# Optimization experiments

Hardware: AMD Instinct MI355X
Metric: run time of the kernel (lower is better)

Reference implementation:

```python
import jax, jax.numpy as jnp
import numpy as np

BG_ID = 0
RADIUS = 10
MODE = 'gauss'
LAMBDA_B = 1.0
GAMMA = 0.1
TEMP = 4.0
EPS = 1e-8
BIG = 1e6  # stands in for +inf (no fg in a row/column); BIG**2 is fp32-safe


def setup_inputs() -> dict:
    key = jax.random.key(0)
    k1, k2 = jax.random.split(key)
    B, C, H, W = 4, 19, 256, 256
    return {
        'student_logits': jax.random.normal(k1, (B, C, H, W), jnp.float32),
        'teacher_logits': jax.random.normal(k2, (B, C, H, W), jnp.float32),
    }


def _edt2(fg):
    """Exact squared Euclidean distance transform of (1 - fg):
    distance from each pixel to the nearest foreground pixel.
    Separable algorithm: 1D column pass (two cumulative scans), then
    exact lower-envelope minimization along rows (vectorized brute force).
    fg: bool [B, H, W]. Returns float32 [B, H, W]."""
    B, H, W = fg.shape
    ii = jnp.arange(H, dtype=jnp.float32)[None, :, None]  # row index
    # 1D vertical distance to nearest fg pixel in each column
    d_fwd = ii - jax.lax.cummax(jnp.where(fg, ii, -BIG), axis=1)
    d_bwd = -jax.lax.cummax(jnp.where(fg, -ii, -BIG), axis=1, reverse=True) - ii
    g = jnp.minimum(jnp.minimum(d_fwd, d_bwd), BIG)  # [B,H,W]
    # exact 2D squared EDT: dist2[b,i,j] = min_{j'} (j-j')^2 + g[b,i,j']^2
    jj = jnp.arange(W, dtype=jnp.float32)
    diff2 = (jj[:, None] - jj[None, :]) ** 2  # [W, W']
    dist2 = jnp.min(diff2[None, None, :, :] + (g * g)[:, :, None, :], axis=-1)
    return dist2


def _erode(fg):
    """scipy.ndimage.binary_erosion with 4-connected cross structure and
    border_value=0 (out-of-bounds treated as background)."""
    p = jnp.pad(fg, ((0, 0), (1, 1), (1, 1)))
    return fg & p[:, :-2, 1:-1] & p[:, 2:, 1:-1] & p[:, 1:-1, :-2] & p[:, 1:-1, 2:]


def _weight_map(teacher_logits):
    # argmax of softmax(probs) == argmax of logits (softmax is monotone per-pixel)
    pred = jnp.argmax(teacher_logits, axis=1)  # [B,H,W]
    fg = pred != BG_ID
    dist2 = _edt2(fg)
    dist = jnp.sqrt(dist2)
    mask = (dist <= RADIUS).astype(jnp.float32)
    sigma = RADIUS / 2.0
    if MODE == 'gauss':
        wdist = jnp.exp(-dist2 / (2.0 * sigma * sigma))
    else:
        wdist = jnp.clip(1.0 - dist / RADIUS, 0.0, 1.0)
    wdist = wdist * mask
    boundary = (fg & ~_erode(fg)).astype(jnp.float32)
    # wb = wdist*(1+lambda_b*boundary); final weights = wb*mask_inside
    # (if an image has no fg pixels, dist is huge -> mask==0 -> weights==0,
    #  matching the scipy loop's `continue` which leaves zeros)
    return wdist * (1.0 + LAMBDA_B * boundary) * mask


def reference(student_logits, teacher_logits):
    weight_map = _weight_map(teacher_logits)  # [B,H,W]
    # teacher probs at temperature T (torch computes t_prob_T and t_prob
    # identically twice; computed once here)
    t_prob = jax.nn.softmax(teacher_logits / TEMP, axis=1)
    entropy = -jnp.sum(t_prob * jnp.log(jnp.clip(t_prob, EPS, None)), axis=1)
    ent_max = jnp.max(entropy, axis=(1, 2), keepdims=True)
    conf_factor = GAMMA + (1.0 - GAMMA) * (1.0 - entropy / (ent_max + EPS))
    s_logp = jax.nn.log_softmax(student_logits / TEMP, axis=1)
    kl_per_pixel = jnp.sum(t_prob * (jnp.log(t_prob + EPS) - s_logp), axis=1)
    total_weight = weight_map * conf_factor
    loss = jnp.sum(total_weight * kl_per_pixel) / (jnp.sum(total_weight) + EPS)
    return TEMP * TEMP * loss
```

## Files before the change

### kernel.cpp

```cpp
#include <hip/hip_runtime.h>
#include <math.h>

#define NC   19
#define HH   256
#define WW   256
#define NB   4
#define HW   (HH * WW)
#define NPIX (NB * HW)
#define CAP2 121.0f

__global__ __launch_bounds__(256) void k_pixel(
    const float* __restrict__ student, const float* __restrict__ teacher,
    float* __restrict__ entropy, float* __restrict__ kl,
    unsigned char* __restrict__ fg, float* __restrict__ bmax)
{
    const int p = blockIdx.x * 256 + threadIdx.x;
    const int b = p >> 16;
    const int r = p & (HW - 1);
    const float* tb = teacher + (size_t)b * NC * HW + r;
    const float* sb = student + (size_t)b * NC * HW + r;

    float St = 0.f, T1 = 0.f, T2 = 0.f, Ss = 0.f;
    float tmx = -INFINITY;
    int ax = 0;
#pragma unroll
    for (int c = 0; c < NC; ++c) {
        float tv = tb[(size_t)c * HW];
        float sv = sb[(size_t)c * HW];
        if (tv > tmx) { tmx = tv; ax = c; }
        float e = __expf(tv * 0.25f);
        St += e;
        T1 += e * tv;
        T2 += e * sv;
        Ss += __expf(sv * 0.25f);
    }
    float rSt = 1.0f / St;
    float ent = __logf(St) - 0.25f * T1 * rSt;
    float klv = __logf(Ss) - 0.25f * T2 * rSt - ent;

    entropy[p] = ent;
    kl[p]      = klv;
    fg[p]      = (ax != 0) ? 1 : 0;

    float m = ent;
#pragma unroll
    for (int o = 32; o >= 1; o >>= 1) m = fmaxf(m, __shfl_down(m, o, 64));
    __shared__ float red[4];
    int wave = threadIdx.x >> 6, lane = threadIdx.x & 63;
    if (lane == 0) red[wave] = m;
    __syncthreads();
    if (threadIdx.x == 0)
        bmax[blockIdx.x] = fmaxf(fmaxf(red[0], red[1]), fmaxf(red[2], red[3]));
}

#define TS   32
#define HALO 10
#define FW   (TS + 2 * HALO)

__global__ __launch_bounds__(256) void k_tile(
    const unsigned char* __restrict__ fg, const float* __restrict__ entropy,
    const float* __restrict__ kl, const float* __restrict__ bmax,
    double* __restrict__ part)
{
    __shared__ float  fgt[FW][FW];
    __shared__ float  vm[TS][FW];
    __shared__ float  red[4];
    __shared__ double snum[4], sden[4];

    const int b   = blockIdx.z;
    const int ti0 = blockIdx.y * TS;
    const int tj0 = blockIdx.x * TS;
    const int tid = threadIdx.x;
    const int wave = tid >> 6, lane = tid & 63;
    const unsigned char* fgb = fg + (size_t)b * HW;

    float m = bmax[(b << 8) + tid];
#pragma unroll
    for (int o = 32; o >= 1; o >>= 1) m = fmaxf(m, __shfl_down(m, o, 64));
    if (lane == 0) red[wave] = m;

    for (int l = tid; l < FW * FW; l += 256) {
        int li = l / FW, lj = l - li * FW;
        int gi = ti0 - HALO + li, gj = tj0 - HALO + lj;
        float v = 0.f;
        if (gi >= 0 && gi < HH && gj >= 0 && gj < WW) v = (float)fgb[gi * WW + gj];
        fgt[li][lj] = v;
    }
    __syncthreads();
    float em = fmaxf(fmaxf(red[0], red[1]), fmaxf(red[2], red[3]));

    for (int l = tid; l < TS * FW; l += 256) {
        int i = l / FW, jj = l - i * FW;
        float mn = CAP2;
#pragma unroll
        for (int di = -HALO; di <= HALO; ++di) {
            float fv = fgt[HALO + i + di][jj];
            mn = fminf(mn, (float)(di * di) + (1.0f - fv) * 1000.0f);
        }
        vm[i][jj] = mn;
    }
    __syncthreads();

    double num = 0.0, den = 0.0;
#pragma unroll
    for (int k = 0; k < (TS * TS) / 256; ++k) {
        int p = tid + k * 256;
        int i = p >> 5, j = p & (TS - 1);
        float d2 = CAP2;
#pragma unroll
        for (int dj = -HALO; dj <= HALO; ++dj)
            d2 = fminf(d2, (float)(dj * dj) + vm[i][j + HALO + dj]);
        float mask  = (d2 <= 100.0f) ? 1.0f : 0.0f;
        float wdist = __expf(-d2 * 0.02f) * mask;

        float f  = fgt[HALO + i][HALO + j];
        float up = fgt[HALO + i - 1][HALO + j];
        float dn = fgt[HALO + i + 1][HALO + j];
        float lf = fgt[HALO + i][HALO + j - 1];
        float rt = fgt[HALO + i][HALO + j + 1];
        float mn4 = fminf(fminf(up, dn), fminf(lf, rt));
        float boundary = (f != 0.f && mn4 == 0.f) ? 1.0f : 0.0f;

        float w = wdist * (1.0f + boundary) * mask;
        size_t gidx = (size_t)b * HW + (size_t)(ti0 + i) * WW + (tj0 + j);
        float conf = 0.1f + 0.9f * (1.0f - entropy[gidx] / (em + 1e-8f));
        float tw = w * conf;
        num += (double)(tw * kl[gidx]);
        den += (double)tw;
    }

#pragma unroll
    for (int o = 32; o >= 1; o >>= 1) {
        num += __shfl_down(num, o, 64);
        den += __shfl_down(den, o, 64);
    }
    if (lane == 0) { snum[wave] = num; sden[wave] = den; }
    __syncthreads();
    if (tid == 0) {
        int bid = (blockIdx.z << 6) + (blockIdx.y << 3) + blockIdx.x;
        part[bid * 2 + 0] = snum[0] + snum[1] + snum[2] + snum[3];
        part[bid * 2 + 1] = sden[0] + sden[1] + sden[2] + sden[3];
    }
}

__global__ __launch_bounds__(256) void k_final(
    const double* __restrict__ part, float* __restrict__ out)
{
    const int tid = threadIdx.x;
    double num = part[tid * 2 + 0];
    double den = part[tid * 2 + 1];
#pragma unroll
    for (int o = 32; o >= 1; o >>= 1) {
        num += __shfl_down(num, o, 64);
        den += __shfl_down(den, o, 64);
    }
    __shared__ double snum[4], sden[4];
    int wave = tid >> 6, lane = tid & 63;
    if (lane == 0) { snum[wave] = num; sden[wave] = den; }
    __syncthreads();
    if (tid == 0) {
        num = snum[0] + snum[1] + snum[2] + snum[3];
        den = sden[0] + sden[1] + sden[2] + sden[3];
        out[0] = (float)(16.0 * num / (den + 1e-8));
    }
}

extern "C" void kernel_launch(void* const* d_in, const int* in_sizes, int n_in,
                              void* d_out, int out_size, void* d_ws, size_t ws_size,
                              hipStream_t stream)
{
    const float* student = (const float*)d_in[0];
    const float* teacher = (const float*)d_in[1];
    float* out = (float*)d_out;

    char* ws = (char*)d_ws;
    double*        part    = (double*)(ws + 0);
    float*         bmax    = (float*)(ws + 8192);
    float*         entropy = (float*)(ws + 16384);
    float*         kl      = (float*)(ws + 16384 + (size_t)NPIX * 4);
    unsigned char* fg      = (unsigned char*)(ws + 16384 + (size_t)NPIX * 8);

    k_pixel<<<NPIX / 256, 256, 0, stream>>>(student, teacher, entropy, kl, fg, bmax);
    dim3 g2(WW / TS, HH / TS, NB);
    k_tile<<<g2, 256, 0, stream>>>(fg, entropy, kl, bmax, part);
    k_final<<<1, 256, 0, stream>>>(part, out);
}
```

Baseline: 88.48 us.

## Vectorize pixel kernel to float4 and widen tile kernel to 512 threads

The per-pixel softmax/KL kernel now has each thread process four adjacent pixels through float4 loads and stores and a uchar4 foreground write, cutting the thread count and issuing wider memory transactions. The tile kernel moves to 512 threads per block, which raises parallelism within its 256 blocks. Its per-image entropy max becomes a single-wave xor-shuffle over the 64 block maxima, removing a shared-memory exchange. Per-thread register use in the pixel kernel grows, which may reduce occupancy there.

```diff
diff --git a/kernel.cpp b/kernel.cpp
--- a/kernel.cpp
+++ b/kernel.cpp
@@ -7,47 +7,68 @@
 #define NB   4
 #define HW   (HH * WW)
 #define NPIX (NB * HW)
+#define NQ   (NPIX / 4)
+#define CHQ  (HW / 4)
 #define CAP2 121.0f
 
 __global__ __launch_bounds__(256) void k_pixel(
-    const float* __restrict__ student, const float* __restrict__ teacher,
-    float* __restrict__ entropy, float* __restrict__ kl,
-    unsigned char* __restrict__ fg, float* __restrict__ bmax)
-{
-    const int p = blockIdx.x * 256 + threadIdx.x;
-    const int b = p >> 16;
-    const int r = p & (HW - 1);
-    const float* tb = teacher + (size_t)b * NC * HW + r;
-    const float* sb = student + (size_t)b * NC * HW + r;
-
-    float St = 0.f, T1 = 0.f, T2 = 0.f, Ss = 0.f;
-    float tmx = -INFINITY;
-    int ax = 0;
+    const float4* __restrict__ student, const float4* __restrict__ teacher,
+    float4* __restrict__ entropy, float4* __restrict__ kl,
+    uchar4* __restrict__ fg, float* __restrict__ bmax)
+{
+    const int q  = blockIdx.x * 256 + threadIdx.x;
+    const int b  = q >> 14;
+    const int rq = q & (CHQ - 1);
+    const float4* tb = teacher + (size_t)b * NC * CHQ + rq;
+    const float4* sb = student + (size_t)b * NC * CHQ + rq;
+
+    float St[4] = {0.f, 0.f, 0.f, 0.f};
+    float T1[4] = {0.f, 0.f, 0.f, 0.f};
+    float T2[4] = {0.f, 0.f, 0.f, 0.f};
+    float Ss[4] = {0.f, 0.f, 0.f, 0.f};
+    float tmx[4] = {-INFINITY, -INFINITY, -INFINITY, -INFINITY};
+    int   ax[4] = {0, 0, 0, 0};
+
 #pragma unroll
     for (int c = 0; c < NC; ++c) {
-        float tv = tb[(size_t)c * HW];
-        float sv = sb[(size_t)c * HW];
-        if (tv > tmx) { tmx = tv; ax = c; }
-        float e = __expf(tv * 0.25f);
-        St += e;
-        T1 += e * tv;
-        T2 += e * sv;
-        Ss += __expf(sv * 0.25f);
-    }
-    float rSt = 1.0f / St;
-    float ent = __logf(St) - 0.25f * T1 * rSt;
-    float klv = __logf(Ss) - 0.25f * T2 * rSt - ent;
-
-    entropy[p] = ent;
-    kl[p]      = klv;
-    fg[p]      = (ax != 0) ? 1 : 0;
-
-    float m = ent;
-#pragma unroll
-    for (int o = 32; o >= 1; o >>= 1) m = fmaxf(m, __shfl_down(m, o, 64));
+        float4 tv4 = tb[(size_t)c * CHQ];
+        float4 sv4 = sb[(size_t)c * CHQ];
+        float tvl[4] = {tv4.x, tv4.y, tv4.z, tv4.w};
+        float svl[4] = {sv4.x, sv4.y, sv4.z, sv4.w};
+#pragma unroll
+        for (int l = 0; l < 4; ++l) {
+            float t = tvl[l], s = svl[l];
+            if (t > tmx[l]) { tmx[l] = t; ax[l] = c; }
+            float e = __expf(t * 0.25f);
+            St[l] += e;
+            T1[l] += e * t;
+            T2[l] += e * s;
+            Ss[l] += __expf(s * 0.25f);
+        }
+    }
+
+    float4 ent4, kl4;
+    uchar4 f4;
+    float em = -INFINITY;
+#pragma unroll
+    for (int l = 0; l < 4; ++l) {
+        float rSt = 1.0f / St[l];
+        float e = __logf(St[l]) - 0.25f * T1[l] * rSt;
+        float k = __logf(Ss[l]) - 0.25f * T2[l] * rSt - e;
+        ((float*)&ent4)[l] = e;
+        ((float*)&kl4)[l]  = k;
+        ((unsigned char*)&f4)[l] = (ax[l] != 0) ? 1 : 0;
+        em = fmaxf(em, e);
+    }
+    entropy[q] = ent4;
+    kl[q]      = kl4;
+    fg[q]      = f4;
+
+#pragma unroll
+    for (int o = 32; o >= 1; o >>= 1) em = fmaxf(em, __shfl_down(em, o, 64));
     __shared__ float red[4];
     int wave = threadIdx.x >> 6, lane = threadIdx.x & 63;
-    if (lane == 0) red[wave] = m;
+    if (lane == 0) red[wave] = em;
     __syncthreads();
     if (threadIdx.x == 0)
         bmax[blockIdx.x] = fmaxf(fmaxf(red[0], red[1]), fmaxf(red[2], red[3]));
@@ -57,15 +78,14 @@
 #define HALO 10
 #define FW   (TS + 2 * HALO)
 
-__global__ __launch_bounds__(256) void k_tile(
+__global__ __launch_bounds__(512) void k_tile(
     const unsigned char* __restrict__ fg, const float* __restrict__ entropy,
     const float* __restrict__ kl, const float* __restrict__ bmax,
     double* __restrict__ part)
 {
     __shared__ float  fgt[FW][FW];
     __shared__ float  vm[TS][FW];
-    __shared__ float  red[4];
-    __shared__ double snum[4], sden[4];
+    __shared__ double snum[8], sden[8];
 
     const int b   = blockIdx.z;
     const int ti0 = blockIdx.y * TS;
@@ -74,12 +94,12 @@
     const int wave = tid >> 6, lane = tid & 63;
     const unsigned char* fgb = fg + (size_t)b * HW;
 
-    float m = bmax[(b << 8) + tid];
-#pragma unroll
-    for (int o = 32; o >= 1; o >>= 1) m = fmaxf(m, __shfl_down(m, o, 64));
-    if (lane == 0) red[wave] = m;
-
-    for (int l = tid; l < FW * FW; l += 256) {
+    float m = bmax[(b << 6) + lane];
+#pragma unroll
+    for (int o = 32; o >= 1; o >>= 1) m = fmaxf(m, __shfl_xor(m, o, 64));
+    const float em = m;
+
+    for (int l = tid; l < FW * FW; l += 512) {
         int li = l / FW, lj = l - li * FW;
         int gi = ti0 - HALO + li, gj = tj0 - HALO + lj;
         float v = 0.f;
@@ -87,9 +107,8 @@
         fgt[li][lj] = v;
     }
     __syncthreads();
-    float em = fmaxf(fmaxf(red[0], red[1]), fmaxf(red[2], red[3]));
-
-    for (int l = tid; l < TS * FW; l += 256) {
+
+    for (int l = tid; l < TS * FW; l += 512) {
         int i = l / FW, jj = l - i * FW;
         float mn = CAP2;
 #pragma unroll
@@ -103,8 +122,8 @@
 
     double num = 0.0, den = 0.0;
 #pragma unroll
-    for (int k = 0; k < (TS * TS) / 256; ++k) {
-        int p = tid + k * 256;
+    for (int k = 0; k < (TS * TS) / 512; ++k) {
+        int p = tid + k * 512;
         int i = p >> 5, j = p & (TS - 1);
         float d2 = CAP2;
 #pragma unroll
@@ -137,9 +156,12 @@
     if (lane == 0) { snum[wave] = num; sden[wave] = den; }
     __syncthreads();
     if (tid == 0) {
+        double n = 0.0, d = 0.0;
+#pragma unroll
+        for (int wv = 0; wv < 8; ++wv) { n += snum[wv]; d += sden[wv]; }
         int bid = (blockIdx.z << 6) + (blockIdx.y << 3) + blockIdx.x;
-        part[bid * 2 + 0] = snum[0] + snum[1] + snum[2] + snum[3];
-        part[bid * 2 + 1] = sden[0] + sden[1] + sden[2] + sden[3];
+        part[bid * 2 + 0] = n;
+        part[bid * 2 + 1] = d;
     }
 }
 
@@ -169,19 +191,21 @@
                               void* d_out, int out_size, void* d_ws, size_t ws_size,
                               hipStream_t stream)
 {
-    const float* student = (const float*)d_in[0];
-    const float* teacher = (const float*)d_in[1];
+    const float4* student = (const float4*)d_in[0];
+    const float4* teacher = (const float4*)d_in[1];
     float* out = (float*)d_out;
 
     char* ws = (char*)d_ws;
     double*        part    = (double*)(ws + 0);
     float*         bmax    = (float*)(ws + 8192);
-    float*         entropy = (float*)(ws + 16384);
-    float*         kl      = (float*)(ws + 16384 + (size_t)NPIX * 4);
-    unsigned char* fg      = (unsigned char*)(ws + 16384 + (size_t)NPIX * 8);
-
-    k_pixel<<<NPIX / 256, 256, 0, stream>>>(student, teacher, entropy, kl, fg, bmax);
+    float4*        entropy = (float4*)(ws + 16384);
+    float4*        kl      = (float4*)(ws + 16384 + (size_t)NPIX * 4);
+    uchar4*        fg      = (uchar4*)(ws + 16384 + (size_t)NPIX * 8);
+
+    k_pixel<<<NQ / 256, 256, 0, stream>>>(student, teacher, entropy, kl, fg, bmax);
     dim3 g2(WW / TS, HH / TS, NB);
-    k_tile<<<g2, 256, 0, stream>>>(fg, entropy, kl, bmax, part);
+    k_tile<<<g2, 512, 0, stream>>>((const unsigned char*)fg,
+                                   (const float*)entropy, (const float*)kl,
+                                   bmax, part);
     k_final<<<1, 256, 0, stream>>>(part, out);
 }
```

Measured after the change: 85.22 us. 3.7% less time.

## Fuse pixel, tile and final reduction into one cooperative kernel

Applied to the files above, without the earlier changes.

Merges the three kernels into a single cooperative launch with 512-thread blocks over 32x32 tiles. Each block computes per-pixel entropy, KL and foreground for its own tile using float2 loads, and keeps entropy and KL in shared memory, so only the foreground byte map goes back to global memory. Two grid-wide syncs stand in for the kernel boundaries: one for the per-image entropy max and halo foreground exchange, one for the final reduction. This removes the global entropy/KL round trip and two launches. In exchange it relies on all 256 blocks being co-resident, adds grid-sync cost, and runs the memory-heavy phase with fewer, larger blocks.

```diff
diff --git a/kernel.cpp b/kernel.cpp
--- a/kernel.cpp
+++ b/kernel.cpp
@@ -1,95 +1,108 @@
 #include <hip/hip_runtime.h>
+#include <hip/hip_cooperative_groups.h>
 #include <math.h>
+
+namespace cg = cooperative_groups;
 
 #define NC   19
 #define HH   256
 #define WW   256
 #define NB   4
 #define HW   (HH * WW)
-#define NPIX (NB * HW)
-#define CAP2 121.0f
-
-__global__ __launch_bounds__(256) void k_pixel(
-    const float* __restrict__ student, const float* __restrict__ teacher,
-    float* __restrict__ entropy, float* __restrict__ kl,
-    unsigned char* __restrict__ fg, float* __restrict__ bmax)
-{
-    const int p = blockIdx.x * 256 + threadIdx.x;
-    const int b = p >> 16;
-    const int r = p & (HW - 1);
-    const float* tb = teacher + (size_t)b * NC * HW + r;
-    const float* sb = student + (size_t)b * NC * HW + r;
-
-    float St = 0.f, T1 = 0.f, T2 = 0.f, Ss = 0.f;
-    float tmx = -INFINITY;
-    int ax = 0;
-#pragma unroll
-    for (int c = 0; c < NC; ++c) {
-        float tv = tb[(size_t)c * HW];
-        float sv = sb[(size_t)c * HW];
-        if (tv > tmx) { tmx = tv; ax = c; }
-        float e = __expf(tv * 0.25f);
-        St += e;
-        T1 += e * tv;
-        T2 += e * sv;
-        Ss += __expf(sv * 0.25f);
-    }
-    float rSt = 1.0f / St;
-    float ent = __logf(St) - 0.25f * T1 * rSt;
-    float klv = __logf(Ss) - 0.25f * T2 * rSt - ent;
-
-    entropy[p] = ent;
-    kl[p]      = klv;
-    fg[p]      = (ax != 0) ? 1 : 0;
-
-    float m = ent;
-#pragma unroll
-    for (int o = 32; o >= 1; o >>= 1) m = fmaxf(m, __shfl_down(m, o, 64));
-    __shared__ float red[4];
-    int wave = threadIdx.x >> 6, lane = threadIdx.x & 63;
-    if (lane == 0) red[wave] = m;
-    __syncthreads();
-    if (threadIdx.x == 0)
-        bmax[blockIdx.x] = fmaxf(fmaxf(red[0], red[1]), fmaxf(red[2], red[3]));
-}
-
 #define TS   32
 #define HALO 10
 #define FW   (TS + 2 * HALO)
+#define CAP2 121.0f
 
-__global__ __launch_bounds__(256) void k_tile(
-    const unsigned char* __restrict__ fg, const float* __restrict__ entropy,
-    const float* __restrict__ kl, const float* __restrict__ bmax,
-    double* __restrict__ part)
+__global__ __launch_bounds__(512) void k_fused(
+    const float* __restrict__ student, const float* __restrict__ teacher,
+    unsigned char* __restrict__ fg, float* __restrict__ bmax,
+    double* __restrict__ part, float* __restrict__ out)
 {
     __shared__ float  fgt[FW][FW];
+    __shared__ float  ent_s[TS][TS];
+    __shared__ float  kl_s[TS][TS];
     __shared__ float  vm[TS][FW];
-    __shared__ float  red[4];
-    __shared__ double snum[4], sden[4];
+    __shared__ float  redf[8];
+    __shared__ double snum[8], sden[8];
 
     const int b   = blockIdx.z;
     const int ti0 = blockIdx.y * TS;
     const int tj0 = blockIdx.x * TS;
     const int tid = threadIdx.x;
     const int wave = tid >> 6, lane = tid & 63;
-    const unsigned char* fgb = fg + (size_t)b * HW;
+    unsigned char* fgb = fg + (size_t)b * HW;
 
-    float m = bmax[(b << 8) + tid];
+    {
+        const int i  = tid >> 4;
+        const int j0 = (tid & 15) << 1;
+        const size_t base = (size_t)b * NC * HW + (size_t)(ti0 + i) * WW + (tj0 + j0);
+        const float2* tp = (const float2*)(teacher + base);
+        const float2* sp = (const float2*)(student + base);
+
+        float St0 = 0.f, St1 = 0.f, T10 = 0.f, T11 = 0.f;
+        float T20 = 0.f, T21 = 0.f, Ss0 = 0.f, Ss1 = 0.f;
+        float tm0 = -INFINITY, tm1 = -INFINITY;
+        int ax0 = 0, ax1 = 0;
 #pragma unroll
-    for (int o = 32; o >= 1; o >>= 1) m = fmaxf(m, __shfl_down(m, o, 64));
-    if (lane == 0) red[wave] = m;
+        for (int c = 0; c < NC; ++c) {
+            float2 tv = tp[(size_t)c * (HW / 2)];
+            float2 sv = sp[(size_t)c * (HW / 2)];
+            if (tv.x > tm0) { tm0 = tv.x; ax0 = c; }
+            float e0 = __expf(tv.x * 0.25f);
+            St0 += e0; T10 += e0 * tv.x; T20 += e0 * sv.x;
+            Ss0 += __expf(sv.x * 0.25f);
+            if (tv.y > tm1) { tm1 = tv.y; ax1 = c; }
+            float e1 = __expf(tv.y * 0.25f);
+            St1 += e1; T11 += e1 * tv.y; T21 += e1 * sv.y;
+            Ss1 += __expf(sv.y * 0.25f);
+        }
+        float r0 = 1.0f / St0, r1 = 1.0f / St1;
+        float e0 = __logf(St0) - 0.25f * T10 * r0;
+        float e1 = __logf(St1) - 0.25f * T11 * r1;
+        float k0 = __logf(Ss0) - 0.25f * T20 * r0 - e0;
+        float k1 = __logf(Ss1) - 0.25f * T21 * r1 - e1;
 
-    for (int l = tid; l < FW * FW; l += 256) {
+        ent_s[i][j0]     = e0;  ent_s[i][j0 + 1] = e1;
+        kl_s[i][j0]      = k0;  kl_s[i][j0 + 1]  = k1;
+        unsigned char f0 = (ax0 != 0) ? 1 : 0;
+        unsigned char f1 = (ax1 != 0) ? 1 : 0;
+        fgt[HALO + i][HALO + j0]     = (float)f0;
+        fgt[HALO + i][HALO + j0 + 1] = (float)f1;
+        uchar2 fpair; fpair.x = f0; fpair.y = f1;
+        *(uchar2*)(fgb + (size_t)(ti0 + i) * WW + (tj0 + j0)) = fpair;
+
+        float em = fmaxf(e0, e1);
+#pragma unroll
+        for (int o = 32; o >= 1; o >>= 1) em = fmaxf(em, __shfl_down(em, o, 64));
+        if (lane == 0) redf[wave] = em;
+        __syncthreads();
+        if (tid == 0) {
+            float mm = redf[0];
+#pragma unroll
+            for (int w = 1; w < 8; ++w) mm = fmaxf(mm, redf[w]);
+            bmax[(b << 6) + (blockIdx.y << 3) + blockIdx.x] = mm;
+        }
+    }
+    __threadfence();
+    cg::this_grid().sync();
+
+    float m = bmax[(b << 6) + lane];
+#pragma unroll
+    for (int o = 32; o >= 1; o >>= 1) m = fmaxf(m, __shfl_xor(m, o, 64));
+    const float em = m;
+
+    for (int l = tid; l < FW * FW; l += 512) {
         int li = l / FW, lj = l - li * FW;
+        if (li >= HALO && li < HALO + TS && lj >= HALO && lj < HALO + TS) continue;
         int gi = ti0 - HALO + li, gj = tj0 - HALO + lj;
         float v = 0.f;
         if (gi >= 0 && gi < HH && gj >= 0 && gj < WW) v = (float)fgb[gi * WW + gj];
         fgt[li][lj] = v;
     }
     __syncthreads();
-    float em = fmaxf(fmaxf(red[0], red[1]), fmaxf(red[2], red[3]));
 
-    for (int l = tid; l < TS * FW; l += 256) {
+    for (int l = tid; l < TS * FW; l += 512) {
         int i = l / FW, jj = l - i * FW;
         float mn = CAP2;
 #pragma unroll
@@ -103,8 +116,8 @@
 
     double num = 0.0, den = 0.0;
 #pragma unroll
-    for (int k = 0; k < (TS * TS) / 256; ++k) {
-        int p = tid + k * 256;
+    for (int k = 0; k < 2; ++k) {
+        int p = tid + k * 512;
         int i = p >> 5, j = p & (TS - 1);
         float d2 = CAP2;
 #pragma unroll
@@ -122,10 +135,9 @@
         float boundary = (f != 0.f && mn4 == 0.f) ? 1.0f : 0.0f;
 
         float w = wdist * (1.0f + boundary) * mask;
-        size_t gidx = (size_t)b * HW + (size_t)(ti0 + i) * WW + (tj0 + j);
-        float conf = 0.1f + 0.9f * (1.0f - entropy[gidx] / (em + 1e-8f));
+        float conf = 0.1f + 0.9f * (1.0f - ent_s[i][j] / (em + 1e-8f));
         float tw = w * conf;
-        num += (double)(tw * kl[gidx]);
+        num += (double)(tw * kl_s[i][j]);
         den += (double)tw;
     }
 
@@ -137,31 +149,31 @@
     if (lane == 0) { snum[wave] = num; sden[wave] = den; }
     __syncthreads();
     if (tid == 0) {
+        double n = 0.0, d = 0.0;
+#pragma unroll
+        for (int w = 0; w < 8; ++w) { n += snum[w]; d += sden[w]; }
         int bid = (blockIdx.z << 6) + (blockIdx.y << 3) + blockIdx.x;
-        part[bid * 2 + 0] = snum[0] + snum[1] + snum[2] + snum[3];
-        part[bid * 2 + 1] = sden[0] + sden[1] + sden[2] + sden[3];
+        part[bid * 2 + 0] = n;
+        part[bid * 2 + 1] = d;
     }
-}
+    __threadfence();
+    cg::this_grid().sync();
 
-__global__ __launch_bounds__(256) void k_final(
-    const double* __restrict__ part, float* __restrict__ out)
-{
-    const int tid = threadIdx.x;
-    double num = part[tid * 2 + 0];
-    double den = part[tid * 2 + 1];
+    if (blockIdx.x == 0 && blockIdx.y == 0 && blockIdx.z == 0) {
+        double n2 = 0.0, d2 = 0.0;
+        if (tid < 256) { n2 = part[tid * 2 + 0]; d2 = part[tid * 2 + 1]; }
 #pragma unroll
-    for (int o = 32; o >= 1; o >>= 1) {
-        num += __shfl_down(num, o, 64);
-        den += __shfl_down(den, o, 64);
-    }
-    __shared__ double snum[4], sden[4];
-    int wave = tid >> 6, lane = tid & 63;
-    if (lane == 0) { snum[wave] = num; sden[wave] = den; }
-    __syncthreads();
-    if (tid == 0) {
-        num = snum[0] + snum[1] + snum[2] + snum[3];
-        den = sden[0] + sden[1] + sden[2] + sden[3];
-        out[0] = (float)(16.0 * num / (den + 1e-8));
+        for (int o = 32; o >= 1; o >>= 1) {
+            n2 += __shfl_down(n2, o, 64);
+            d2 += __shfl_down(d2, o, 64);
+        }
+        if (lane == 0) { snum[wave] = n2; sden[wave] = d2; }
+        __syncthreads();
+        if (tid == 0) {
+            double n = snum[0] + snum[1] + snum[2] + snum[3];
+            double d = sden[0] + sden[1] + sden[2] + sden[3];
+            out[0] = (float)(16.0 * n / (d + 1e-8));
+        }
     }
 }
 
@@ -174,14 +186,13 @@
     float* out = (float*)d_out;
 
     char* ws = (char*)d_ws;
-    double*        part    = (double*)(ws + 0);
-    float*         bmax    = (float*)(ws + 8192);
-    float*         entropy = (float*)(ws + 16384);
-    float*         kl      = (float*)(ws + 16384 + (size_t)NPIX * 4);
-    unsigned char* fg      = (unsigned char*)(ws + 16384 + (size_t)NPIX * 8);
+    double*        part = (double*)(ws + 0);
+    float*         bmax = (float*)(ws + 8192);
+    unsigned char* fg   = (unsigned char*)(ws + 16384);
 
-    k_pixel<<<NPIX / 256, 256, 0, stream>>>(student, teacher, entropy, kl, fg, bmax);
-    dim3 g2(WW / TS, HH / TS, NB);
-    k_tile<<<g2, 256, 0, stream>>>(fg, entropy, kl, bmax, part);
-    k_final<<<1, 256, 0, stream>>>(part, out);
+    dim3 grid(WW / TS, HH / TS, NB);
+    dim3 block(512);
+    void* args[] = { (void*)&student, (void*)&teacher, (void*)&fg,
+                     (void*)&bmax, (void*)&part, (void*)&out };
+    hipLaunchCooperativeKernel((const void*)k_fused, grid, block, args, 0, stream);
 }
```

New measurement: 204.1 us. +130.6%, slower.
